# Optimization experiments

Measured on AMD Instinct MI355X. Metric: run time of the kernel, lower is better.

Reference implementation:

```python
import jax, jax.numpy as jnp
import numpy as np

N_EMBD = 1024
N_HEAD = 16
HEAD_DIM = N_EMBD // N_HEAD


def _linear_params(key, fan_in, fan_out):
    kw, kb = jax.random.split(key)
    bound = 1.0 / np.sqrt(fan_in)
    W = jax.random.uniform(kw, (fan_out, fan_in), minval=-bound, maxval=bound, dtype=jnp.float32)
    b = jax.random.uniform(kb, (fan_out,), minval=-bound, maxval=bound, dtype=jnp.float32)
    return W, b


def setup_inputs() -> dict:
    key = jax.random.key(0)
    ks = jax.random.split(key, 7)
    B, T, C = 4, 2048, N_EMBD
    k = jax.random.normal(ks[0], (B, T, C), dtype=jnp.float32)
    q = jax.random.normal(ks[1], (B, T, C), dtype=jnp.float32)
    v = jax.random.normal(ks[2], (B, T, C), dtype=jnp.float32)
    Wk, bk = _linear_params(ks[3], C, C)
    Wq, bq = _linear_params(ks[4], C, C)
    Wv, bv = _linear_params(ks[5], C, C)
    Wo, bo = _linear_params(ks[6], C, C)
    return {"k": k, "q": q, "v": v, "Wk": Wk, "bk": bk, "Wq": Wq, "bq": bq,
            "Wv": Wv, "bv": bv, "Wo": Wo, "bo": bo}


def reference(k, q, v, Wk, bk, Wq, bq, Wv, bv, Wo, bo):
    B, T, C = k.shape
    H, CH = N_HEAD, C // N_HEAD
    # projections (nn.Linear: x @ W.T + b), split heads -> [b, h, t, ch]
    keys = (k @ Wk.T + bk).reshape(B, T, H, CH).transpose(0, 2, 1, 3)
    queries = (q @ Wq.T + bq).reshape(B, T, H, CH).transpose(0, 2, 1, 3)
    values = (v @ Wv.T + bv).reshape(B, T, H, CH).transpose(0, 2, 1, 3)
    # [b, h, t, t] scores, scaled before softmax as in the original
    att = jnp.einsum('bhqd,bhkd->bhqk', queries, keys)
    att = jax.nn.softmax(att * (CH ** -0.5), axis=-1)
    out = jnp.einsum('bhqk,bhkd->bhqd', att, values)
    out = out.transpose(0, 2, 1, 3).reshape(B, T, C)
    return out @ Wo.T + bo
```

## Files before the change

### kernel.cpp

```cpp
#include <hip/hip_runtime.h>


typedef short bf8 __attribute__((ext_vector_type(8)));
typedef float f4 __attribute__((ext_vector_type(4)));
typedef float f16v __attribute__((ext_vector_type(16)));
typedef unsigned short u16;

#define AS1 __attribute__((address_space(1)))
#define AS3 __attribute__((address_space(3)))

__device__ __forceinline__ u16 f2b(float f) {
  unsigned u = __builtin_bit_cast(unsigned, f);
  u += 0x7FFFu + ((u >> 16) & 1u);
  return (u16)(u >> 16);
}

__device__ __forceinline__ unsigned cvtpk(float lo, float hi) {
  unsigned r;
  asm("v_cvt_pk_bf16_f32 %0, %1, %2" : "=v"(r) : "v"(lo), "v"(hi));
  return r;
}

__device__ __forceinline__ void swap32(unsigned& a, unsigned& b) {
  asm("v_permlane32_swap_b32 %0, %1" : "+v"(a), "+v"(b));
}

__global__ void cvt4_kernel(const float* __restrict__ a, const float* __restrict__ b,
                            const float* __restrict__ c, const float* __restrict__ d,
                            u16* __restrict__ out) {
  int i = blockIdx.x * blockDim.x + threadIdx.x;
  const int sel = i >> 18, off = i & 0x3FFFF;
  const float* src = sel == 0 ? a : sel == 1 ? b : sel == 2 ? c : d;
  float4 f = ((const float4*)src)[off];
  ushort4 o;
  o.x = f2b(f.x); o.y = f2b(f.y); o.z = f2b(f.z); o.w = f2b(f.w);
  ((ushort4*)out)[i] = o;
}

template<int MODE>
__device__ __forceinline__ void gemm_epilogue(
    f4 (&acc)[4][4], const float* __restrict__ bias, void* __restrict__ Cout,
    int N, float scale, int m0, int n0, int wm, int wn, int lr, int lg)
{
  if (MODE == 0) {
    float bv[4];
    #pragma unroll
    for (int j = 0; j < 4; ++j) bv[j] = bias[n0 + wn + j * 16 + lr];
    float* C = (float*)Cout;
    #pragma unroll
    for (int i = 0; i < 4; ++i)
      #pragma unroll
      for (int j = 0; j < 4; ++j) {
        const int col = n0 + wn + j * 16 + lr;
        #pragma unroll
        for (int r = 0; r < 4; ++r) {
          const int row = m0 + wm + i * 16 + lg * 4 + r;
          C[(size_t)row * N + col] = acc[i][j][r] + bv[j];
        }
      }
  } else if (MODE == 1) {
    float bv[4];
    #pragma unroll
    for (int j = 0; j < 4; ++j) bv[j] = bias[n0 + wn + j * 16 + lr];
    u16* C = (u16*)Cout;
    #pragma unroll
    for (int i = 0; i < 4; ++i)
      #pragma unroll
      for (int j = 0; j < 4; ++j) {
        const int col = n0 + wn + j * 16 + lr;
        const int h = col >> 6, ch = col & 63;
        #pragma unroll
        for (int r = 0; r < 4; ++r) {
          const int row = m0 + wm + i * 16 + lg * 4 + r;
          const int b = row >> 11, t = row & 2047;
          C[((size_t)(b * 16 + h) * 2048 + t) * 64 + ch] = f2b((acc[i][j][r] + bv[j]) * scale);
        }
      }
  } else {
    u16* C = (u16*)Cout;
    #pragma unroll
    for (int i = 0; i < 4; ++i)
      #pragma unroll
      for (int r = 0; r < 4; ++r) {
        const int nch = m0 + wm + i * 16 + lg * 4 + r;
        const float br = bias[nch];
        const int h = nch >> 6, ch = nch & 63;
        #pragma unroll
        for (int j = 0; j < 4; ++j) {
          const int tok = n0 + wn + j * 16 + lr;
          const int b = tok >> 11, t = tok & 2047;
          C[((size_t)((b * 16 + h) * 64 + ch) << 11) + t] = f2b(acc[i][j][r] + br);
        }
      }
  }
}

template<int MODE, int ACTB>
__device__ __forceinline__ void gemm_fp_body(
    u16* __restrict__ actT, u16* __restrict__ wT,
    const float* __restrict__ act, const u16* __restrict__ Wt,
    const float* __restrict__ bias, void* __restrict__ Cout,
    int N, int K, float scale, int m0, int n0)
{
  const int tid = threadIdx.x, lane = tid & 63, w = tid >> 6;
  const int wm = (w >> 1) << 6, wn = (w & 1) << 6;
  const int lr = lane & 15, lg = lane >> 4;
  const int arow0 = (ACTB ? n0 : m0);
  const int wrow0 = (ACTB ? m0 : n0);

  f4 acc[4][4] = {};
  float4 ta[8];

  #define W_GLDS(buf, karg)                                                     \
    do {                                                                        \
      const int k_ = (karg);                                                    \
      u16* dst = wT + ((buf) << 13);                                            \
      _Pragma("unroll")                                                         \
      for (int q = 0; q < 4; ++q) {                                             \
        const int c = (w << 8) + (q << 6) + lane;                               \
        const int row = c >> 3, sw = ((c & 7) ^ (row & 7)) << 3;                \
        __builtin_amdgcn_global_load_lds(                                       \
            (const AS1 void*)(Wt + (size_t)(wrow0 + row) * K + k_ + sw),        \
            (AS3 void*)(dst + (((w << 2) + q) << 9)), 16, 0, 0);                \
      }                                                                         \
    } while (0)

  #define ACT_LOAD(karg)                                                        \
    do {                                                                        \
      const int k_ = (karg);                                                    \
      _Pragma("unroll")                                                         \
      for (int q = 0; q < 4; ++q) {                                             \
        const int c = (w << 8) + (q << 6) + lane;                               \
        const int row = c >> 3, col = (c & 7) << 3;                             \
        const float* s = act + (size_t)(arow0 + row) * K + k_ + col;            \
        ta[2 * q] = *(const float4*)s;                                          \
        ta[2 * q + 1] = *(const float4*)(s + 4);                                \
      }                                                                         \
    } while (0)

  #define ACT_WRITE(buf)                                                        \
    do {                                                                        \
      u16* dst = actT + ((buf) << 13);                                          \
      _Pragma("unroll")                                                         \
      for (int q = 0; q < 4; ++q) {                                             \
        const int c = (w << 8) + (q << 6) + lane;                               \
        const int row = c >> 3;                                                 \
        uint4 pk;                                                               \
        pk.x = cvtpk(ta[2 * q].x, ta[2 * q].y);                                 \
        pk.y = cvtpk(ta[2 * q].z, ta[2 * q].w);                                 \
        pk.z = cvtpk(ta[2 * q + 1].x, ta[2 * q + 1].y);                         \
        pk.w = cvtpk(ta[2 * q + 1].z, ta[2 * q + 1].w);                         \
        *(uint4*)(dst + (row << 6) + (((c & 7) ^ (row & 7)) << 3)) = pk;        \
      }                                                                         \
    } while (0)

  W_GLDS(0, 0);
  ACT_LOAD(0);
  ACT_WRITE(0);
  ACT_LOAD(64);
  asm volatile("s_waitcnt lgkmcnt(0)" ::: "memory");

  const int NKT = K >> 6;
  for (int kt = 0; kt < NKT; ++kt) {
    const int cur = kt & 1;
    if (kt > 0) {
      if (kt + 1 < NKT) asm volatile("s_waitcnt vmcnt(8)" ::: "memory");
      else              asm volatile("s_waitcnt vmcnt(0)" ::: "memory");
    }
    __builtin_amdgcn_s_barrier();
    __builtin_amdgcn_sched_barrier(0);

    if (kt + 1 < NKT) W_GLDS(cur ^ 1, (kt + 1) << 6);

    const u16* aC = actT + (cur << 13);
    const u16* wC = wT + (cur << 13);
    #pragma unroll
    for (int ks = 0; ks < 2; ++ks) {
      bf8 af[4], bfr[4];
      #pragma unroll
      for (int i = 0; i < 4; ++i) {
        const int ra = wm + i * 16 + lr;
        const int rb = wn + i * 16 + lr;
        const u16* aSrc = ACTB ? wC : aC;
        const u16* bSrc = ACTB ? aC : wC;
        af[i]  = *(const bf8*)(aSrc + (ra << 6) + ((((ks << 2) + lg) ^ (ra & 7)) << 3));
        bfr[i] = *(const bf8*)(bSrc + (rb << 6) + ((((ks << 2) + lg) ^ (rb & 7)) << 3));
      }
      __builtin_amdgcn_s_setprio(1);
      #pragma unroll
      for (int i = 0; i < 4; ++i)
        #pragma unroll
        for (int j = 0; j < 4; ++j)
          acc[i][j] = __builtin_amdgcn_mfma_f32_16x16x32_bf16(af[i], bfr[j], acc[i][j], 0, 0, 0);
      __builtin_amdgcn_s_setprio(0);
    }

    if (kt + 1 < NKT) {
      ACT_WRITE(cur ^ 1);
      if (kt + 2 < NKT) ACT_LOAD((kt + 2) << 6);
    }
    asm volatile("s_waitcnt lgkmcnt(0)" ::: "memory");
  }
  #undef W_GLDS
  #undef ACT_LOAD
  #undef ACT_WRITE

  gemm_epilogue<MODE>(acc, bias, Cout, N, scale, m0, n0, wm, wn, lr, lg);
}

__global__ __launch_bounds__(256, 2)
void proj_qkv(const float* __restrict__ q_in, const float* __restrict__ k_in,
              const float* __restrict__ v_in,
              const u16* __restrict__ Wq, const u16* __restrict__ Wk,
              const u16* __restrict__ Wv,
              const float* __restrict__ bq, const float* __restrict__ bk,
              const float* __restrict__ bv,
              u16* __restrict__ Qp, u16* __restrict__ Kp, u16* __restrict__ Vt,
              float qscale)
{
  __shared__ __align__(16) u16 pool[32768];
  u16* const actT = pool;
  u16* const wT   = pool + 16384;

  const int cpx = gridDim.x >> 3;
  const int bid = (blockIdx.x & 7) * cpx + (blockIdx.x >> 3);
  const int which = bid >> 9, sub = bid & 511;

  if (which < 2) {
    gemm_fp_body<1, 0>(actT, wT,
                       which ? k_in : q_in,
                       which ? Wk : Wq,
                       which ? bk : bq,
                       which ? (void*)Kp : (void*)Qp,
                       1024, 1024, which ? 1.f : qscale,
                       (sub >> 3) << 7, (sub & 7) << 7);
  } else {
    gemm_fp_body<2, 1>(actT, wT, v_in, Wv, bv, (void*)Vt,
                       8192, 1024, 1.f, (sub & 7) << 7, (sub >> 3) << 7);
  }
}

__global__ __launch_bounds__(256, 2)
void gemm_out(const u16* __restrict__ A, const u16* __restrict__ B,
              const float* __restrict__ bias, float* __restrict__ C)
{
  __shared__ __align__(16) u16 pool[32768];
  u16* const aT = pool;
  u16* const bT = pool + 16384;

  const int cpx = gridDim.x >> 3;
  const int bid = (blockIdx.x & 7) * cpx + (blockIdx.x >> 3);
  const int m0 = (bid >> 3) << 7, n0 = (bid & 7) << 7;
  const int tid = threadIdx.x, lane = tid & 63, w = tid >> 6;
  const int wm = (w >> 1) << 6, wn = (w & 1) << 6;
  const int lr = lane & 15, lg = lane >> 4;
  const int K = 1024;

  f4 acc[4][4] = {};

  #pragma unroll
  for (int q = 0; q < 4; ++q) {
    const int c = (w << 8) + (q << 6) + lane;
    const int row = c >> 3, sw = ((c & 7) ^ (row & 7)) << 3;
    __builtin_amdgcn_global_load_lds(
        (const AS1 void*)(A + (size_t)(m0 + row) * K + sw),
        (AS3 void*)(aT + (((w << 2) + q) << 9)), 16, 0, 0);
    __builtin_amdgcn_global_load_lds(
        (const AS1 void*)(B + (size_t)(n0 + row) * K + sw),
        (AS3 void*)(bT + (((w << 2) + q) << 9)), 16, 0, 0);
  }
  __syncthreads();

  for (int kt = 0; kt < 16; ++kt) {
    const int cur = kt & 1;
    const u16* aC = aT + (cur << 13);
    const u16* bC = bT + (cur << 13);
    if (kt + 1 < 16) {
      u16* aN = aT + ((cur ^ 1) << 13);
      u16* bN = bT + ((cur ^ 1) << 13);
      const int k1 = (kt + 1) << 6;
      #pragma unroll
      for (int q = 0; q < 4; ++q) {
        const int c = (w << 8) + (q << 6) + lane;
        const int row = c >> 3, sw = ((c & 7) ^ (row & 7)) << 3;
        __builtin_amdgcn_global_load_lds(
            (const AS1 void*)(A + (size_t)(m0 + row) * K + k1 + sw),
            (AS3 void*)(aN + (((w << 2) + q) << 9)), 16, 0, 0);
        __builtin_amdgcn_global_load_lds(
            (const AS1 void*)(B + (size_t)(n0 + row) * K + k1 + sw),
            (AS3 void*)(bN + (((w << 2) + q) << 9)), 16, 0, 0);
      }
    }
    #pragma unroll
    for (int ks = 0; ks < 2; ++ks) {
      bf8 af[4], bfr[4];
      #pragma unroll
      for (int i = 0; i < 4; ++i) {
        const int ra = wm + i * 16 + lr;
        const int rb = wn + i * 16 + lr;
        af[i]  = *(const bf8*)(aC + (ra << 6) + ((((ks << 2) + lg) ^ (ra & 7)) << 3));
        bfr[i] = *(const bf8*)(bC + (rb << 6) + ((((ks << 2) + lg) ^ (rb & 7)) << 3));
      }
      __builtin_amdgcn_s_setprio(1);
      #pragma unroll
      for (int i = 0; i < 4; ++i)
        #pragma unroll
        for (int j = 0; j < 4; ++j)
          acc[i][j] = __builtin_amdgcn_mfma_f32_16x16x32_bf16(af[i], bfr[j], acc[i][j], 0, 0, 0);
      __builtin_amdgcn_s_setprio(0);
    }
    __syncthreads();
  }

  gemm_epilogue<0>(acc, bias, (void*)C, 1024, 1.f, m0, n0, wm, wn, lr, lg);
}

__global__ __launch_bounds__(256, 3)
void attn_kernel(const u16* __restrict__ Qp, const u16* __restrict__ Kp,
                 const u16* __restrict__ VT, u16* __restrict__ Ob)
{
  __shared__ __align__(16) u16 pool[24576];
  u16* const ktb = pool;
  u16* const vtb = pool + 12288;

  const int flat = blockIdx.x;
  const int xcd = flat & 7, idx = flat >> 3;
  const int bh = (xcd << 3) + (idx >> 4);
  const int tq0 = (idx & 15) << 7;

  const int tid = threadIdx.x, lane = tid & 63, w = tid >> 6;
  const int ql = lane & 31, hi = lane >> 5;
  const size_t hoff = (size_t)bh * (2048 * 64);
  const u16* Kh = Kp + hoff;
  const u16* Vh = VT + hoff;

  bf8 qf[4];
  {
    const u16* qp_ = Qp + hoff + (size_t)(tq0 + w * 32 + ql) * 64 + hi * 8;
    #pragma unroll
    for (int ks = 0; ks < 4; ++ks) qf[ks] = *(const bf8*)(qp_ + 16 * ks);
  }

  f16v o0 = {}, o1 = {};
  float lrun = 0.f;

  const int c0i = (w << 7) + lane;
  const int c1i = c0i + 64;
  const int sr0 = c0i >> 3, ss0 = ((c0i & 7) ^ (sr0 & 7)) << 3;
  const int sr1 = c1i >> 3, ss1 = ((c1i & 7) ^ (sr1 & 7)) << 3;
  const int sd0 = (w << 10);
  const int sd1 = (w << 10) + 512;

  #define STAGE(buf, t0)                                                          \
    do {                                                                           \
      __builtin_amdgcn_global_load_lds((const AS1 void*)(Kh + (size_t)((t0) + sr0) * 64 + ss0), \
                                       (AS3 void*)(ktb + (buf) * 4096 + sd0), 16, 0, 0);  \
      __builtin_amdgcn_global_load_lds((const AS1 void*)(Kh + (size_t)((t0) + sr1) * 64 + ss1), \
                                       (AS3 void*)(ktb + (buf) * 4096 + sd1), 16, 0, 0);  \
      __builtin_amdgcn_global_load_lds((const AS1 void*)(Vh + (size_t)sr0 * 2048 + (t0) + ss0), \
                                       (AS3 void*)(vtb + (buf) * 4096 + sd0), 16, 0, 0);  \
      __builtin_amdgcn_global_load_lds((const AS1 void*)(Vh + (size_t)sr1 * 2048 + (t0) + ss1), \
                                       (AS3 void*)(vtb + (buf) * 4096 + sd1), 16, 0, 0);  \
    } while (0)

  STAGE(0, 0);
  STAGE(1, 64);

  const int xq = ql & 7;
  int bc = 0;
  for (int it = 0; it < 32; ++it) {
    if (it < 31) asm volatile("s_waitcnt vmcnt(4)" ::: "memory");
    else         asm volatile("s_waitcnt vmcnt(0)" ::: "memory");
    __builtin_amdgcn_s_barrier();
    __builtin_amdgcn_sched_barrier(0);

    if (it + 2 < 32) {
      const int bs = bc ? bc - 1 : 2;
      STAGE(bs, (it + 2) << 6);
    }

    const u16* kb = ktb + bc * 4096;
    const u16* vb = vtb + bc * 4096;

    f16v s0 = {}, s1 = {};
    #pragma unroll
    for (int ks = 0; ks < 4; ++ks) {
      bf8 kf0 = *(const bf8*)(kb + (ql << 6) + ((((ks << 1) + hi) ^ xq) << 3));
      bf8 kf1 = *(const bf8*)(kb + ((32 + ql) << 6) + ((((ks << 1) + hi) ^ xq) << 3));
      __builtin_amdgcn_s_setprio(1);
      s0 = __builtin_amdgcn_mfma_f32_32x32x16_bf16(kf0, qf[ks], s0, 0, 0, 0);
      s1 = __builtin_amdgcn_mfma_f32_32x32x16_bf16(kf1, qf[ks], s1, 0, 0, 0);
      __builtin_amdgcn_s_setprio(0);
    }

    bf8 vf0[4], vf1[4];
    #pragma unroll
    for (int ks = 0; ks < 4; ++ks) {
      vf0[ks] = *(const bf8*)(vb + (ql << 6) + ((((ks << 1) + hi) ^ xq) << 3));
      vf1[ks] = *(const bf8*)(vb + ((32 + ql) << 6) + ((((ks << 1) + hi) ^ xq) << 3));
    }

    float rs = 0.f;

    {
      unsigned wpk[8];
      #pragma unroll
      for (int i = 0; i < 8; ++i) {
        float e0 = __builtin_amdgcn_exp2f(s0[2 * i]);
        float e1 = __builtin_amdgcn_exp2f(s0[2 * i + 1]);
        rs += e0 + e1;
        wpk[i] = cvtpk(e0, e1);
      }
      swap32(wpk[0], wpk[2]); swap32(wpk[1], wpk[3]);
      swap32(wpk[4], wpk[6]); swap32(wpk[5], wpk[7]);
      bf8 pf0 = __builtin_bit_cast(bf8, make_uint4(wpk[0], wpk[1], wpk[2], wpk[3]));
      bf8 pf1 = __builtin_bit_cast(bf8, make_uint4(wpk[4], wpk[5], wpk[6], wpk[7]));
      __builtin_amdgcn_s_setprio(1);
      o0 = __builtin_amdgcn_mfma_f32_32x32x16_bf16(vf0[0], pf0, o0, 0, 0, 0);
      o1 = __builtin_amdgcn_mfma_f32_32x32x16_bf16(vf1[0], pf0, o1, 0, 0, 0);
      o0 = __builtin_amdgcn_mfma_f32_32x32x16_bf16(vf0[1], pf1, o0, 0, 0, 0);
      o1 = __builtin_amdgcn_mfma_f32_32x32x16_bf16(vf1[1], pf1, o1, 0, 0, 0);
      __builtin_amdgcn_s_setprio(0);
    }

    {
      unsigned wpk[8];
      #pragma unroll
      for (int i = 0; i < 8; ++i) {
        float e0 = __builtin_amdgcn_exp2f(s1[2 * i]);
        float e1 = __builtin_amdgcn_exp2f(s1[2 * i + 1]);
        rs += e0 + e1;
        wpk[i] = cvtpk(e0, e1);
      }
      swap32(wpk[0], wpk[2]); swap32(wpk[1], wpk[3]);
      swap32(wpk[4], wpk[6]); swap32(wpk[5], wpk[7]);
      bf8 pf2 = __builtin_bit_cast(bf8, make_uint4(wpk[0], wpk[1], wpk[2], wpk[3]));
      bf8 pf3 = __builtin_bit_cast(bf8, make_uint4(wpk[4], wpk[5], wpk[6], wpk[7]));
      __builtin_amdgcn_s_setprio(1);
      o0 = __builtin_amdgcn_mfma_f32_32x32x16_bf16(vf0[2], pf2, o0, 0, 0, 0);
      o1 = __builtin_amdgcn_mfma_f32_32x32x16_bf16(vf1[2], pf2, o1, 0, 0, 0);
      o0 = __builtin_amdgcn_mfma_f32_32x32x16_bf16(vf0[3], pf3, o0, 0, 0, 0);
      o1 = __builtin_amdgcn_mfma_f32_32x32x16_bf16(vf1[3], pf3, o1, 0, 0, 0);
      __builtin_amdgcn_s_setprio(0);
    }

    lrun += rs;
    bc = bc + 1 < 3 ? bc + 1 : 0;
  }
  #undef STAGE

  const float linv = 1.f / (lrun + __shfl_xor(lrun, 32));

  __syncthreads();
  u16* const ot = pool;
  const int orow = w * 32 + ql;
  #pragma unroll
  for (int c = 0; c < 2; ++c) {
    const f16v& o = c ? o1 : o0;
    #pragma unroll
    for (int g = 0; g < 4; ++g) {
      uint2 pk;
      pk.x = cvtpk(o[4 * g + 0] * linv, o[4 * g + 1] * linv);
      pk.y = cvtpk(o[4 * g + 2] * linv, o[4 * g + 3] * linv);
      *(uint2*)(ot + orow * 72 + 32 * c + 8 * g + 4 * hi) = pk;
    }
  }
  __syncthreads();

  const int b = bh >> 4, h = bh & 15;
  const int row = tid >> 1, seg = tid & 1;
  const u16* src = ot + row * 72 + seg * 32;
  u16* dst = Ob + ((size_t)(b * 2048 + tq0 + row) * 16 + h) * 64 + seg * 32;
  #pragma unroll
  for (int kk = 0; kk < 4; ++kk)
    *(uint4*)(dst + 8 * kk) = *(const uint4*)(src + 8 * kk);
}

extern "C" void kernel_launch(void* const* d_in, const int* in_sizes, int n_in,
                              void* d_out, int out_size, void* d_ws, size_t ws_size,
                              hipStream_t stream) {
  (void)in_sizes; (void)n_in; (void)out_size; (void)ws_size;
  const float* k_in = (const float*)d_in[0];
  const float* q_in = (const float*)d_in[1];
  const float* v_in = (const float*)d_in[2];
  const float* Wk = (const float*)d_in[3]; const float* bk = (const float*)d_in[4];
  const float* Wq = (const float*)d_in[5]; const float* bq = (const float*)d_in[6];
  const float* Wv = (const float*)d_in[7]; const float* bv = (const float*)d_in[8];
  const float* Wo = (const float*)d_in[9]; const float* bo = (const float*)d_in[10];
  float* out = (float*)d_out;

  char* ws = (char*)d_ws;
  const size_t SZ_ACT = (size_t)8192 * 1024 * 2;
  const size_t SZ_W   = (size_t)1024 * 1024 * 2;
  u16* Oc  = (u16*)(ws);
  u16* Qp  = (u16*)(ws + 1 * SZ_ACT);
  u16* Kp  = (u16*)(ws + 2 * SZ_ACT);
  u16* Vt  = (u16*)(ws + 3 * SZ_ACT);
  u16* Wqb = (u16*)(ws + 4 * SZ_ACT);
  u16* Wkb = (u16*)(ws + 4 * SZ_ACT + SZ_W);
  u16* Wvb = (u16*)(ws + 4 * SZ_ACT + 2 * SZ_W);
  u16* Wob = (u16*)(ws + 4 * SZ_ACT + 3 * SZ_W);

  cvt4_kernel<<<4096, 256, 0, stream>>>(Wq, Wk, Wv, Wo, Wqb);

  const float c0 = 0.125f * 1.4426950408889634f;

  proj_qkv<<<1536, 256, 0, stream>>>(q_in, k_in, v_in, Wqb, Wkb, Wvb,
                                     bq, bk, bv, Qp, Kp, Vt, c0);

  attn_kernel<<<1024, 256, 0, stream>>>(Qp, Kp, Vt, Oc);

  gemm_out<<<512, 256, 0, stream>>>(Oc, Wob, bo, out);
}
```

Measured before the change: 179.1 us.

## Shrink projection GEMM K-tile to 32 with triple-buffered LDS for higher occupancy

Reworks the fused QKV projection GEMM to use a K-tile of 32 instead of 64. It uses three LDS buffers instead of two, with a new 4-way swizzle and a new per-thread load mapping. LDS per block drops from 64KB to 48KB and the activation register staging is halved, so launch bounds go from 2 to 3 blocks per CU. The cost is twice as many barriers and K iterations, and less MFMA work between each synchronization.

```diff
diff --git a/kernel.cpp b/kernel.cpp
--- a/kernel.cpp
+++ b/kernel.cpp
@@ -107,84 +107,89 @@
   const int lr = lane & 15, lg = lane >> 4;
   const int arow0 = (ACTB ? n0 : m0);
   const int wrow0 = (ACTB ? m0 : n0);
+  const int aloc  = (ACTB ? wn : wm);
+  const int wloc  = (ACTB ? wm : wn);
 
   f4 acc[4][4] = {};
-  float4 ta[8];
+  float4 ta[4];
+
+  const int wq0row = (w << 5) + (lane >> 2);
+  const int wq1row = wq0row + 16;
+  const int wx = lane & 3;
+  const int ws0 = (wx ^ (wq0row & 3)) << 3;
+  const int ws1 = (wx ^ (wq1row & 3)) << 3;
+  const int wd0 = (w << 10);
+  const int wd1 = (w << 10) + 512;
+
+  const int ar   = tid >> 1;
+  const int axh  = (tid & 1) << 4;
+  const int ax0  = (tid & 1) << 1;
+  const int asw0 = ((ax0 ^ (ar & 3)) << 3);
+  const int asw1 = (((ax0 | 1) ^ (ar & 3)) << 3);
+  const int abase = ar << 5;
 
   #define W_GLDS(buf, karg)                                                     \
     do {                                                                        \
       const int k_ = (karg);                                                    \
-      u16* dst = wT + ((buf) << 13);                                            \
-      _Pragma("unroll")                                                         \
-      for (int q = 0; q < 4; ++q) {                                             \
-        const int c = (w << 8) + (q << 6) + lane;                               \
-        const int row = c >> 3, sw = ((c & 7) ^ (row & 7)) << 3;                \
-        __builtin_amdgcn_global_load_lds(                                       \
-            (const AS1 void*)(Wt + (size_t)(wrow0 + row) * K + k_ + sw),        \
-            (AS3 void*)(dst + (((w << 2) + q) << 9)), 16, 0, 0);                \
-      }                                                                         \
+      u16* dst = wT + (buf) * 4096;                                             \
+      __builtin_amdgcn_global_load_lds(                                         \
+          (const AS1 void*)(Wt + (size_t)(wrow0 + wq0row) * K + k_ + ws0),      \
+          (AS3 void*)(dst + wd0), 16, 0, 0);                                    \
+      __builtin_amdgcn_global_load_lds(                                         \
+          (const AS1 void*)(Wt + (size_t)(wrow0 + wq1row) * K + k_ + ws1),      \
+          (AS3 void*)(dst + wd1), 16, 0, 0);                                    \
     } while (0)
 
   #define ACT_LOAD(karg)                                                        \
     do {                                                                        \
-      const int k_ = (karg);                                                    \
-      _Pragma("unroll")                                                         \
-      for (int q = 0; q < 4; ++q) {                                             \
-        const int c = (w << 8) + (q << 6) + lane;                               \
-        const int row = c >> 3, col = (c & 7) << 3;                             \
-        const float* s = act + (size_t)(arow0 + row) * K + k_ + col;            \
-        ta[2 * q] = *(const float4*)s;                                          \
-        ta[2 * q + 1] = *(const float4*)(s + 4);                                \
-      }                                                                         \
+      const float* s = act + (size_t)(arow0 + ar) * K + (karg) + axh;           \
+      ta[0] = *(const float4*)(s);                                              \
+      ta[1] = *(const float4*)(s + 4);                                          \
+      ta[2] = *(const float4*)(s + 8);                                          \
+      ta[3] = *(const float4*)(s + 12);                                         \
     } while (0)
 
   #define ACT_WRITE(buf)                                                        \
     do {                                                                        \
-      u16* dst = actT + ((buf) << 13);                                          \
-      _Pragma("unroll")                                                         \
-      for (int q = 0; q < 4; ++q) {                                             \
-        const int c = (w << 8) + (q << 6) + lane;                               \
-        const int row = c >> 3;                                                 \
-        uint4 pk;                                                               \
-        pk.x = cvtpk(ta[2 * q].x, ta[2 * q].y);                                 \
-        pk.y = cvtpk(ta[2 * q].z, ta[2 * q].w);                                 \
-        pk.z = cvtpk(ta[2 * q + 1].x, ta[2 * q + 1].y);                         \
-        pk.w = cvtpk(ta[2 * q + 1].z, ta[2 * q + 1].w);                         \
-        *(uint4*)(dst + (row << 6) + (((c & 7) ^ (row & 7)) << 3)) = pk;        \
-      }                                                                         \
+      u16* dst = actT + (buf) * 4096 + abase;                                   \
+      uint4 pk0, pk1;                                                           \
+      pk0.x = cvtpk(ta[0].x, ta[0].y); pk0.y = cvtpk(ta[0].z, ta[0].w);         \
+      pk0.z = cvtpk(ta[1].x, ta[1].y); pk0.w = cvtpk(ta[1].z, ta[1].w);         \
+      pk1.x = cvtpk(ta[2].x, ta[2].y); pk1.y = cvtpk(ta[2].z, ta[2].w);         \
+      pk1.z = cvtpk(ta[3].x, ta[3].y); pk1.w = cvtpk(ta[3].z, ta[3].w);         \
+      *(uint4*)(dst + asw0) = pk0;                                              \
+      *(uint4*)(dst + asw1) = pk1;                                              \
     } while (0)
 
+  ACT_LOAD(0);
   W_GLDS(0, 0);
-  ACT_LOAD(0);
   ACT_WRITE(0);
-  ACT_LOAD(64);
+  ACT_LOAD(32);
   asm volatile("s_waitcnt lgkmcnt(0)" ::: "memory");
 
-  const int NKT = K >> 6;
+  const int NKT = K >> 5;
+  int bc = 0;
   for (int kt = 0; kt < NKT; ++kt) {
-    const int cur = kt & 1;
-    if (kt > 0) {
-      if (kt + 1 < NKT) asm volatile("s_waitcnt vmcnt(8)" ::: "memory");
-      else              asm volatile("s_waitcnt vmcnt(0)" ::: "memory");
-    }
+    if (kt + 1 < NKT) asm volatile("s_waitcnt vmcnt(4)" ::: "memory");
+    else              asm volatile("s_waitcnt vmcnt(0)" ::: "memory");
     __builtin_amdgcn_s_barrier();
     __builtin_amdgcn_sched_barrier(0);
 
-    if (kt + 1 < NKT) W_GLDS(cur ^ 1, (kt + 1) << 6);
-
-    const u16* aC = actT + (cur << 13);
-    const u16* wC = wT + (cur << 13);
-    #pragma unroll
-    for (int ks = 0; ks < 2; ++ks) {
+    const int bn = bc == 2 ? 0 : bc + 1;
+    if (kt + 1 < NKT) W_GLDS(bn, (kt + 1) << 5);
+
+    const u16* aC = actT + bc * 4096;
+    const u16* wC = wT + bc * 4096;
+    {
       bf8 af[4], bfr[4];
       #pragma unroll
       for (int i = 0; i < 4; ++i) {
-        const int ra = wm + i * 16 + lr;
-        const int rb = wn + i * 16 + lr;
-        const u16* aSrc = ACTB ? wC : aC;
-        const u16* bSrc = ACTB ? aC : wC;
-        af[i]  = *(const bf8*)(aSrc + (ra << 6) + ((((ks << 2) + lg) ^ (ra & 7)) << 3));
-        bfr[i] = *(const bf8*)(bSrc + (rb << 6) + ((((ks << 2) + lg) ^ (rb & 7)) << 3));
+        const int ral = aloc + i * 16 + lr;
+        const int rwl = wloc + i * 16 + lr;
+        const bf8 actf = *(const bf8*)(aC + (ral << 5) + ((lg ^ (ral & 3)) << 3));
+        const bf8 wf   = *(const bf8*)(wC + (rwl << 5) + ((lg ^ (rwl & 3)) << 3));
+        af[i]  = ACTB ? wf : actf;
+        bfr[i] = ACTB ? actf : wf;
       }
       __builtin_amdgcn_s_setprio(1);
       #pragma unroll
@@ -196,10 +201,11 @@
     }
 
     if (kt + 1 < NKT) {
-      ACT_WRITE(cur ^ 1);
-      if (kt + 2 < NKT) ACT_LOAD((kt + 2) << 6);
+      ACT_WRITE(bn);
+      if (kt + 2 < NKT) ACT_LOAD((kt + 2) << 5);
     }
     asm volatile("s_waitcnt lgkmcnt(0)" ::: "memory");
+    bc = bn;
   }
   #undef W_GLDS
   #undef ACT_LOAD
@@ -208,7 +214,7 @@
   gemm_epilogue<MODE>(acc, bias, Cout, N, scale, m0, n0, wm, wn, lr, lg);
 }
 
-__global__ __launch_bounds__(256, 2)
+__global__ __launch_bounds__(256, 3)
 void proj_qkv(const float* __restrict__ q_in, const float* __restrict__ k_in,
               const float* __restrict__ v_in,
               const u16* __restrict__ Wq, const u16* __restrict__ Wk,
@@ -218,9 +224,9 @@
               u16* __restrict__ Qp, u16* __restrict__ Kp, u16* __restrict__ Vt,
               float qscale)
 {
-  __shared__ __align__(16) u16 pool[32768];
+  __shared__ __align__(16) u16 pool[24576];
   u16* const actT = pool;
-  u16* const wT   = pool + 16384;
+  u16* const wT   = pool + 12288;
 
   const int cpx = gridDim.x >> 3;
   const int bid = (blockIdx.x & 7) * cpx + (blockIdx.x >> 3);
```

After: 188.9 us. +5.5%, slower.

## Software-pipeline QK^T of next tile with softmax/PV of current tile

Applied to the files above, without the earlier changes.

Restructures the attention inner loop so the QK^T MFMAs for tile t+1 are issued before the exp/pack/PV work for tile t, using ping-pong score registers unrolled by two. The goal is to overlap matrix-core work with the transcendental and permute work of the softmax. In exchange it holds two extra 32x32 accumulators, which raises register pressure at 3 waves per SIMD. It also now waits on vmcnt(0) every iteration, which weakens the overlap of global-to-LDS prefetch.

```diff
diff --git a/kernel.cpp b/kernel.cpp
--- a/kernel.cpp
+++ b/kernel.cpp
@@ -315,6 +315,72 @@
   gemm_epilogue<0>(acc, bias, (void*)C, 1024, 1.f, m0, n0, wm, wn, lr, lg);
 }
 
+__device__ __forceinline__ void qk_tile(const u16* kb, const bf8 (&qf)[4],
+                                        int ql, int hi, int xq, f16v& s0, f16v& s1) {
+  #pragma unroll
+  for (int ks = 0; ks < 4; ++ks) {
+    bf8 kf0 = *(const bf8*)(kb + (ql << 6) + ((((ks << 1) + hi) ^ xq) << 3));
+    bf8 kf1 = *(const bf8*)(kb + ((32 + ql) << 6) + ((((ks << 1) + hi) ^ xq) << 3));
+    __builtin_amdgcn_s_setprio(1);
+    s0 = __builtin_amdgcn_mfma_f32_32x32x16_bf16(kf0, qf[ks], s0, 0, 0, 0);
+    s1 = __builtin_amdgcn_mfma_f32_32x32x16_bf16(kf1, qf[ks], s1, 0, 0, 0);
+    __builtin_amdgcn_s_setprio(0);
+  }
+}
+
+__device__ __forceinline__ void sm_pv(f16v& s0v, f16v& s1v, const u16* vb,
+                                      int ql, int hi, int xq,
+                                      f16v& o0, f16v& o1, float& lrun) {
+  bf8 vf0[4], vf1[4];
+  #pragma unroll
+  for (int ks = 0; ks < 4; ++ks) {
+    vf0[ks] = *(const bf8*)(vb + (ql << 6) + ((((ks << 1) + hi) ^ xq) << 3));
+    vf1[ks] = *(const bf8*)(vb + ((32 + ql) << 6) + ((((ks << 1) + hi) ^ xq) << 3));
+  }
+  float rs = 0.f;
+  {
+    unsigned wpk[8];
+    #pragma unroll
+    for (int i = 0; i < 8; ++i) {
+      float e0 = __builtin_amdgcn_exp2f(s0v[2 * i]);
+      float e1 = __builtin_amdgcn_exp2f(s0v[2 * i + 1]);
+      rs += e0 + e1;
+      wpk[i] = cvtpk(e0, e1);
+    }
+    swap32(wpk[0], wpk[2]); swap32(wpk[1], wpk[3]);
+    swap32(wpk[4], wpk[6]); swap32(wpk[5], wpk[7]);
+    bf8 pf0 = __builtin_bit_cast(bf8, make_uint4(wpk[0], wpk[1], wpk[2], wpk[3]));
+    bf8 pf1 = __builtin_bit_cast(bf8, make_uint4(wpk[4], wpk[5], wpk[6], wpk[7]));
+    __builtin_amdgcn_s_setprio(1);
+    o0 = __builtin_amdgcn_mfma_f32_32x32x16_bf16(vf0[0], pf0, o0, 0, 0, 0);
+    o1 = __builtin_amdgcn_mfma_f32_32x32x16_bf16(vf1[0], pf0, o1, 0, 0, 0);
+    o0 = __builtin_amdgcn_mfma_f32_32x32x16_bf16(vf0[1], pf1, o0, 0, 0, 0);
+    o1 = __builtin_amdgcn_mfma_f32_32x32x16_bf16(vf1[1], pf1, o1, 0, 0, 0);
+    __builtin_amdgcn_s_setprio(0);
+  }
+  {
+    unsigned wpk[8];
+    #pragma unroll
+    for (int i = 0; i < 8; ++i) {
+      float e0 = __builtin_amdgcn_exp2f(s1v[2 * i]);
+      float e1 = __builtin_amdgcn_exp2f(s1v[2 * i + 1]);
+      rs += e0 + e1;
+      wpk[i] = cvtpk(e0, e1);
+    }
+    swap32(wpk[0], wpk[2]); swap32(wpk[1], wpk[3]);
+    swap32(wpk[4], wpk[6]); swap32(wpk[5], wpk[7]);
+    bf8 pf2 = __builtin_bit_cast(bf8, make_uint4(wpk[0], wpk[1], wpk[2], wpk[3]));
+    bf8 pf3 = __builtin_bit_cast(bf8, make_uint4(wpk[4], wpk[5], wpk[6], wpk[7]));
+    __builtin_amdgcn_s_setprio(1);
+    o0 = __builtin_amdgcn_mfma_f32_32x32x16_bf16(vf0[2], pf2, o0, 0, 0, 0);
+    o1 = __builtin_amdgcn_mfma_f32_32x32x16_bf16(vf1[2], pf2, o1, 0, 0, 0);
+    o0 = __builtin_amdgcn_mfma_f32_32x32x16_bf16(vf0[3], pf3, o0, 0, 0, 0);
+    o1 = __builtin_amdgcn_mfma_f32_32x32x16_bf16(vf1[3], pf3, o1, 0, 0, 0);
+    __builtin_amdgcn_s_setprio(0);
+  }
+  lrun += rs;
+}
+
 __global__ __launch_bounds__(256, 3)
 void attn_kernel(const u16* __restrict__ Qp, const u16* __restrict__ Kp,
                  const u16* __restrict__ VT, u16* __restrict__ Ob)
@@ -342,6 +408,7 @@
   }
 
   f16v o0 = {}, o1 = {};
+  f16v sA0 = {}, sA1 = {}, sB0 = {}, sB1 = {};
   float lrun = 0.f;
 
   const int c0i = (w << 7) + lane;
@@ -363,90 +430,37 @@
                                        (AS3 void*)(vtb + (buf) * 4096 + sd1), 16, 0, 0);  \
     } while (0)
 
+  const int xq = ql & 7;
+
   STAGE(0, 0);
   STAGE(1, 64);
-
-  const int xq = ql & 7;
+  asm volatile("s_waitcnt vmcnt(4)" ::: "memory");
+  __builtin_amdgcn_s_barrier();
+  qk_tile(ktb, qf, ql, hi, xq, sA0, sA1);
+
   int bc = 0;
-  for (int it = 0; it < 32; ++it) {
-    if (it < 31) asm volatile("s_waitcnt vmcnt(4)" ::: "memory");
-    else         asm volatile("s_waitcnt vmcnt(0)" ::: "memory");
-    __builtin_amdgcn_s_barrier();
-    __builtin_amdgcn_sched_barrier(0);
-
-    if (it + 2 < 32) {
-      const int bs = bc ? bc - 1 : 2;
-      STAGE(bs, (it + 2) << 6);
-    }
-
-    const u16* kb = ktb + bc * 4096;
-    const u16* vb = vtb + bc * 4096;
-
-    f16v s0 = {}, s1 = {};
-    #pragma unroll
-    for (int ks = 0; ks < 4; ++ks) {
-      bf8 kf0 = *(const bf8*)(kb + (ql << 6) + ((((ks << 1) + hi) ^ xq) << 3));
-      bf8 kf1 = *(const bf8*)(kb + ((32 + ql) << 6) + ((((ks << 1) + hi) ^ xq) << 3));
-      __builtin_amdgcn_s_setprio(1);
-      s0 = __builtin_amdgcn_mfma_f32_32x32x16_bf16(kf0, qf[ks], s0, 0, 0, 0);
-      s1 = __builtin_amdgcn_mfma_f32_32x32x16_bf16(kf1, qf[ks], s1, 0, 0, 0);
-      __builtin_amdgcn_s_setprio(0);
-    }
-
-    bf8 vf0[4], vf1[4];
-    #pragma unroll
-    for (int ks = 0; ks < 4; ++ks) {
-      vf0[ks] = *(const bf8*)(vb + (ql << 6) + ((((ks << 1) + hi) ^ xq) << 3));
-      vf1[ks] = *(const bf8*)(vb + ((32 + ql) << 6) + ((((ks << 1) + hi) ^ xq) << 3));
-    }
-
-    float rs = 0.f;
-
-    {
-      unsigned wpk[8];
-      #pragma unroll
-      for (int i = 0; i < 8; ++i) {
-        float e0 = __builtin_amdgcn_exp2f(s0[2 * i]);
-        float e1 = __builtin_amdgcn_exp2f(s0[2 * i + 1]);
-        rs += e0 + e1;
-        wpk[i] = cvtpk(e0, e1);
-      }
-      swap32(wpk[0], wpk[2]); swap32(wpk[1], wpk[3]);
-      swap32(wpk[4], wpk[6]); swap32(wpk[5], wpk[7]);
-      bf8 pf0 = __builtin_bit_cast(bf8, make_uint4(wpk[0], wpk[1], wpk[2], wpk[3]));
-      bf8 pf1 = __builtin_bit_cast(bf8, make_uint4(wpk[4], wpk[5], wpk[6], wpk[7]));
-      __builtin_amdgcn_s_setprio(1);
-      o0 = __builtin_amdgcn_mfma_f32_32x32x16_bf16(vf0[0], pf0, o0, 0, 0, 0);
-      o1 = __builtin_amdgcn_mfma_f32_32x32x16_bf16(vf1[0], pf0, o1, 0, 0, 0);
-      o0 = __builtin_amdgcn_mfma_f32_32x32x16_bf16(vf0[1], pf1, o0, 0, 0, 0);
-      o1 = __builtin_amdgcn_mfma_f32_32x32x16_bf16(vf1[1], pf1, o1, 0, 0, 0);
-      __builtin_amdgcn_s_setprio(0);
-    }
-
-    {
-      unsigned wpk[8];
-      #pragma unroll
-      for (int i = 0; i < 8; ++i) {
-        float e0 = __builtin_amdgcn_exp2f(s1[2 * i]);
-        float e1 = __builtin_amdgcn_exp2f(s1[2 * i + 1]);
-        rs += e0 + e1;
-        wpk[i] = cvtpk(e0, e1);
-      }
-      swap32(wpk[0], wpk[2]); swap32(wpk[1], wpk[3]);
-      swap32(wpk[4], wpk[6]); swap32(wpk[5], wpk[7]);
-      bf8 pf2 = __builtin_bit_cast(bf8, make_uint4(wpk[0], wpk[1], wpk[2], wpk[3]));
-      bf8 pf3 = __builtin_bit_cast(bf8, make_uint4(wpk[4], wpk[5], wpk[6], wpk[7]));
-      __builtin_amdgcn_s_setprio(1);
-      o0 = __builtin_amdgcn_mfma_f32_32x32x16_bf16(vf0[2], pf2, o0, 0, 0, 0);
-      o1 = __builtin_amdgcn_mfma_f32_32x32x16_bf16(vf1[2], pf2, o1, 0, 0, 0);
-      o0 = __builtin_amdgcn_mfma_f32_32x32x16_bf16(vf0[3], pf3, o0, 0, 0, 0);
-      o1 = __builtin_amdgcn_mfma_f32_32x32x16_bf16(vf1[3], pf3, o1, 0, 0, 0);
-      __builtin_amdgcn_s_setprio(0);
-    }
-
-    lrun += rs;
-    bc = bc + 1 < 3 ? bc + 1 : 0;
-  }
+  #define BODY(sc0, sc1, sn0, sn1, T)                                            \
+    do {                                                                          \
+      const int t_ = (T);                                                         \
+      asm volatile("s_waitcnt vmcnt(0)" ::: "memory");                            \
+      __builtin_amdgcn_s_barrier();                                               \
+      __builtin_amdgcn_sched_barrier(0);                                          \
+      const int bn_ = bc + 1 < 3 ? bc + 1 : 0;                                    \
+      const int bs_ = bn_ + 1 < 3 ? bn_ + 1 : 0;                                  \
+      if (t_ + 2 < 32) STAGE(bs_, (t_ + 2) << 6);                                 \
+      if (t_ + 1 < 32) {                                                          \
+        sn0 = (f16v){}; sn1 = (f16v){};                                           \
+        qk_tile(ktb + bn_ * 4096, qf, ql, hi, xq, sn0, sn1);                      \
+      }                                                                           \
+      sm_pv(sc0, sc1, vtb + bc * 4096, ql, hi, xq, o0, o1, lrun);                 \
+      bc = bn_;                                                                   \
+    } while (0)
+
+  for (int tt = 0; tt < 16; ++tt) {
+    BODY(sA0, sA1, sB0, sB1, 2 * tt);
+    BODY(sB0, sB1, sA0, sA1, 2 * tt + 1);
+  }
+  #undef BODY
   #undef STAGE
 
   const float linv = 1.f / (lrun + __shfl_xor(lrun, 32));
```

Result: no change. 179.3 us (+0.2%).

## Pre-convert activations to bf16 and unify projection GEMMs on direct LDS loads

Applied to the files above, without the earlier changes.

Adds a single conversion kernel that turns the q/k/v activations, as well as the weights, into bf16 workspace buffers. The QKV projection then loads both operands through global-to-LDS copies with a simple double-buffered loop, and shares one GEMM body with the output projection. This removes the in-register fp32 load-and-convert path and its custom waitcnt pipelining. In exchange it adds an extra full pass writing and re-reading the activations in bf16, and uses more workspace.

```diff
diff --git a/kernel.cpp b/kernel.cpp
--- a/kernel.cpp
+++ b/kernel.cpp
@@ -25,16 +25,30 @@
   asm("v_permlane32_swap_b32 %0, %1" : "+v"(a), "+v"(b));
 }
 
-__global__ void cvt4_kernel(const float* __restrict__ a, const float* __restrict__ b,
-                            const float* __restrict__ c, const float* __restrict__ d,
-                            u16* __restrict__ out) {
-  int i = blockIdx.x * blockDim.x + threadIdx.x;
-  const int sel = i >> 18, off = i & 0x3FFFF;
-  const float* src = sel == 0 ? a : sel == 1 ? b : sel == 2 ? c : d;
-  float4 f = ((const float4*)src)[off];
+__global__ void cvt_all(const float* __restrict__ q, const float* __restrict__ k,
+                        const float* __restrict__ v,
+                        const float* __restrict__ Wq_, const float* __restrict__ Wk_,
+                        const float* __restrict__ Wv_, const float* __restrict__ Wo_,
+                        u16* __restrict__ qb, u16* __restrict__ kb,
+                        u16* __restrict__ vb, u16* __restrict__ wb) {
+  const int i = blockIdx.x * blockDim.x + threadIdx.x;
+  float4 f;
   ushort4 o;
-  o.x = f2b(f.x); o.y = f2b(f.y); o.z = f2b(f.z); o.w = f2b(f.w);
-  ((ushort4*)out)[i] = o;
+  if (i < (1 << 20)) {
+    const int s = i >> 18, off = i & 0x3FFFF;
+    const float* src = s == 0 ? Wq_ : s == 1 ? Wk_ : s == 2 ? Wv_ : Wo_;
+    f = ((const float4*)src)[off];
+    o.x = f2b(f.x); o.y = f2b(f.y); o.z = f2b(f.z); o.w = f2b(f.w);
+    ((ushort4*)wb)[i] = o;
+  } else {
+    const int j = i - (1 << 20);
+    const int s = j >> 21, off = j & 0x1FFFFF;
+    const float* src = s == 0 ? q : s == 1 ? k : v;
+    u16* dst = s == 0 ? qb : s == 1 ? kb : vb;
+    f = ((const float4*)src)[off];
+    o.x = f2b(f.x); o.y = f2b(f.y); o.z = f2b(f.z); o.w = f2b(f.w);
+    ((ushort4*)dst)[off] = o;
+  }
 }
 
 template<int MODE>
@@ -95,85 +109,47 @@
   }
 }
 
-template<int MODE, int ACTB>
-__device__ __forceinline__ void gemm_fp_body(
-    u16* __restrict__ actT, u16* __restrict__ wT,
-    const float* __restrict__ act, const u16* __restrict__ Wt,
+template<int MODE>
+__device__ __forceinline__ void gemm_bf16_body(
+    u16* __restrict__ aT, u16* __restrict__ bT,
+    const u16* __restrict__ A, const u16* __restrict__ B,
     const float* __restrict__ bias, void* __restrict__ Cout,
     int N, int K, float scale, int m0, int n0)
 {
   const int tid = threadIdx.x, lane = tid & 63, w = tid >> 6;
   const int wm = (w >> 1) << 6, wn = (w & 1) << 6;
   const int lr = lane & 15, lg = lane >> 4;
-  const int arow0 = (ACTB ? n0 : m0);
-  const int wrow0 = (ACTB ? m0 : n0);
 
   f4 acc[4][4] = {};
-  float4 ta[8];
-
-  #define W_GLDS(buf, karg)                                                     \
+
+  #define AB_STAGE(buf, karg)                                                   \
     do {                                                                        \
       const int k_ = (karg);                                                    \
-      u16* dst = wT + ((buf) << 13);                                            \
+      u16* da = aT + ((buf) << 13);                                             \
+      u16* db = bT + ((buf) << 13);                                             \
       _Pragma("unroll")                                                         \
       for (int q = 0; q < 4; ++q) {                                             \
         const int c = (w << 8) + (q << 6) + lane;                               \
         const int row = c >> 3, sw = ((c & 7) ^ (row & 7)) << 3;                \
         __builtin_amdgcn_global_load_lds(                                       \
-            (const AS1 void*)(Wt + (size_t)(wrow0 + row) * K + k_ + sw),        \
-            (AS3 void*)(dst + (((w << 2) + q) << 9)), 16, 0, 0);                \
+            (const AS1 void*)(A + (size_t)(m0 + row) * K + k_ + sw),            \
+            (AS3 void*)(da + (((w << 2) + q) << 9)), 16, 0, 0);                 \
+        __builtin_amdgcn_global_load_lds(                                       \
+            (const AS1 void*)(B + (size_t)(n0 + row) * K + k_ + sw),            \
+            (AS3 void*)(db + (((w << 2) + q) << 9)), 16, 0, 0);                 \
       }                                                                         \
     } while (0)
 
-  #define ACT_LOAD(karg)                                                        \
-    do {                                                                        \
-      const int k_ = (karg);                                                    \
-      _Pragma("unroll")                                                         \
-      for (int q = 0; q < 4; ++q) {                                             \
-        const int c = (w << 8) + (q << 6) + lane;                               \
-        const int row = c >> 3, col = (c & 7) << 3;                             \
-        const float* s = act + (size_t)(arow0 + row) * K + k_ + col;            \
-        ta[2 * q] = *(const float4*)s;                                          \
-        ta[2 * q + 1] = *(const float4*)(s + 4);                                \
-      }                                                                         \
-    } while (0)
-
-  #define ACT_WRITE(buf)                                                        \
-    do {                                                                        \
-      u16* dst = actT + ((buf) << 13);                                          \
-      _Pragma("unroll")                                                         \
-      for (int q = 0; q < 4; ++q) {                                             \
-        const int c = (w << 8) + (q << 6) + lane;                               \
-        const int row = c >> 3;                                                 \
-        uint4 pk;                                                               \
-        pk.x = cvtpk(ta[2 * q].x, ta[2 * q].y);                                 \
-        pk.y = cvtpk(ta[2 * q].z, ta[2 * q].w);                                 \
-        pk.z = cvtpk(ta[2 * q + 1].x, ta[2 * q + 1].y);                         \
-        pk.w = cvtpk(ta[2 * q + 1].z, ta[2 * q + 1].w);                         \
-        *(uint4*)(dst + (row << 6) + (((c & 7) ^ (row & 7)) << 3)) = pk;        \
-      }                                                                         \
-    } while (0)
-
-  W_GLDS(0, 0);
-  ACT_LOAD(0);
-  ACT_WRITE(0);
-  ACT_LOAD(64);
-  asm volatile("s_waitcnt lgkmcnt(0)" ::: "memory");
+  AB_STAGE(0, 0);
+  __syncthreads();
 
   const int NKT = K >> 6;
   for (int kt = 0; kt < NKT; ++kt) {
     const int cur = kt & 1;
-    if (kt > 0) {
-      if (kt + 1 < NKT) asm volatile("s_waitcnt vmcnt(8)" ::: "memory");
-      else              asm volatile("s_waitcnt vmcnt(0)" ::: "memory");
-    }
-    __builtin_amdgcn_s_barrier();
-    __builtin_amdgcn_sched_barrier(0);
-
-    if (kt + 1 < NKT) W_GLDS(cur ^ 1, (kt + 1) << 6);
-
-    const u16* aC = actT + (cur << 13);
-    const u16* wC = wT + (cur << 13);
+    const u16* aC = aT + (cur << 13);
+    const u16* bC = bT + (cur << 13);
+    if (kt + 1 < NKT) AB_STAGE(cur ^ 1, (kt + 1) << 6);
+
     #pragma unroll
     for (int ks = 0; ks < 2; ++ks) {
       bf8 af[4], bfr[4];
@@ -181,10 +157,8 @@
       for (int i = 0; i < 4; ++i) {
         const int ra = wm + i * 16 + lr;
         const int rb = wn + i * 16 + lr;
-        const u16* aSrc = ACTB ? wC : aC;
-        const u16* bSrc = ACTB ? aC : wC;
-        af[i]  = *(const bf8*)(aSrc + (ra << 6) + ((((ks << 2) + lg) ^ (ra & 7)) << 3));
-        bfr[i] = *(const bf8*)(bSrc + (rb << 6) + ((((ks << 2) + lg) ^ (rb & 7)) << 3));
+        af[i]  = *(const bf8*)(aC + (ra << 6) + ((((ks << 2) + lg) ^ (ra & 7)) << 3));
+        bfr[i] = *(const bf8*)(bC + (rb << 6) + ((((ks << 2) + lg) ^ (rb & 7)) << 3));
       }
       __builtin_amdgcn_s_setprio(1);
       #pragma unroll
@@ -194,23 +168,16 @@
           acc[i][j] = __builtin_amdgcn_mfma_f32_16x16x32_bf16(af[i], bfr[j], acc[i][j], 0, 0, 0);
       __builtin_amdgcn_s_setprio(0);
     }
-
-    if (kt + 1 < NKT) {
-      ACT_WRITE(cur ^ 1);
-      if (kt + 2 < NKT) ACT_LOAD((kt + 2) << 6);
-    }
-    asm volatile("s_waitcnt lgkmcnt(0)" ::: "memory");
-  }
-  #undef W_GLDS
-  #undef ACT_LOAD
-  #undef ACT_WRITE
+    __syncthreads();
+  }
+  #undef AB_STAGE
 
   gemm_epilogue<MODE>(acc, bias, Cout, N, scale, m0, n0, wm, wn, lr, lg);
 }
 
 __global__ __launch_bounds__(256, 2)
-void proj_qkv(const float* __restrict__ q_in, const float* __restrict__ k_in,
-              const float* __restrict__ v_in,
+void proj_qkv(const u16* __restrict__ qb, const u16* __restrict__ kb,
+              const u16* __restrict__ vb,
               const u16* __restrict__ Wq, const u16* __restrict__ Wk,
               const u16* __restrict__ Wv,
               const float* __restrict__ bq, const float* __restrict__ bk,
@@ -219,24 +186,24 @@
               float qscale)
 {
   __shared__ __align__(16) u16 pool[32768];
-  u16* const actT = pool;
-  u16* const wT   = pool + 16384;
+  u16* const aT = pool;
+  u16* const bT = pool + 16384;
 
   const int cpx = gridDim.x >> 3;
   const int bid = (blockIdx.x & 7) * cpx + (blockIdx.x >> 3);
   const int which = bid >> 9, sub = bid & 511;
 
   if (which < 2) {
-    gemm_fp_body<1, 0>(actT, wT,
-                       which ? k_in : q_in,
-                       which ? Wk : Wq,
-                       which ? bk : bq,
-                       which ? (void*)Kp : (void*)Qp,
-                       1024, 1024, which ? 1.f : qscale,
-                       (sub >> 3) << 7, (sub & 7) << 7);
+    gemm_bf16_body<1>(aT, bT,
+                      which ? kb : qb,
+                      which ? Wk : Wq,
+                      which ? bk : bq,
+                      which ? (void*)Kp : (void*)Qp,
+                      1024, 1024, which ? 1.f : qscale,
+                      (sub >> 3) << 7, (sub & 7) << 7);
   } else {
-    gemm_fp_body<2, 1>(actT, wT, v_in, Wv, bv, (void*)Vt,
-                       8192, 1024, 1.f, (sub & 7) << 7, (sub >> 3) << 7);
+    gemm_bf16_body<2>(aT, bT, Wv, vb, bv, (void*)Vt,
+                      8192, 1024, 1.f, (sub & 7) << 7, (sub >> 3) << 7);
   }
 }
 
@@ -250,69 +217,8 @@
 
   const int cpx = gridDim.x >> 3;
   const int bid = (blockIdx.x & 7) * cpx + (blockIdx.x >> 3);
-  const int m0 = (bid >> 3) << 7, n0 = (bid & 7) << 7;
-  const int tid = threadIdx.x, lane = tid & 63, w = tid >> 6;
-  const int wm = (w >> 1) << 6, wn = (w & 1) << 6;
-  const int lr = lane & 15, lg = lane >> 4;
-  const int K = 1024;
-
-  f4 acc[4][4] = {};
-
-  #pragma unroll
-  for (int q = 0; q < 4; ++q) {
-    const int c = (w << 8) + (q << 6) + lane;
-    const int row = c >> 3, sw = ((c & 7) ^ (row & 7)) << 3;
-    __builtin_amdgcn_global_load_lds(
-        (const AS1 void*)(A + (size_t)(m0 + row) * K + sw),
-        (AS3 void*)(aT + (((w << 2) + q) << 9)), 16, 0, 0);
-    __builtin_amdgcn_global_load_lds(
-        (const AS1 void*)(B + (size_t)(n0 + row) * K + sw),
-        (AS3 void*)(bT + (((w << 2) + q) << 9)), 16, 0, 0);
-  }
-  __syncthreads();
-
-  for (int kt = 0; kt < 16; ++kt) {
-    const int cur = kt & 1;
-    const u16* aC = aT + (cur << 13);
-    const u16* bC = bT + (cur << 13);
-    if (kt + 1 < 16) {
-      u16* aN = aT + ((cur ^ 1) << 13);
-      u16* bN = bT + ((cur ^ 1) << 13);
-      const int k1 = (kt + 1) << 6;
-      #pragma unroll
-      for (int q = 0; q < 4; ++q) {
-        const int c = (w << 8) + (q << 6) + lane;
-        const int row = c >> 3, sw = ((c & 7) ^ (row & 7)) << 3;
-        __builtin_amdgcn_global_load_lds(
-            (const AS1 void*)(A + (size_t)(m0 + row) * K + k1 + sw),
-            (AS3 void*)(aN + (((w << 2) + q) << 9)), 16, 0, 0);
-        __builtin_amdgcn_global_load_lds(
-            (const AS1 void*)(B + (size_t)(n0 + row) * K + k1 + sw),
-            (AS3 void*)(bN + (((w << 2) + q) << 9)), 16, 0, 0);
-      }
-    }
-    #pragma unroll
-    for (int ks = 0; ks < 2; ++ks) {
-      bf8 af[4], bfr[4];
-      #pragma unroll
-      for (int i = 0; i < 4; ++i) {
-        const int ra = wm + i * 16 + lr;
-        const int rb = wn + i * 16 + lr;
-        af[i]  = *(const bf8*)(aC + (ra << 6) + ((((ks << 2) + lg) ^ (ra & 7)) << 3));
-        bfr[i] = *(const bf8*)(bC + (rb << 6) + ((((ks << 2) + lg) ^ (rb & 7)) << 3));
-      }
-      __builtin_amdgcn_s_setprio(1);
-      #pragma unroll
-      for (int i = 0; i < 4; ++i)
-        #pragma unroll
-        for (int j = 0; j < 4; ++j)
-          acc[i][j] = __builtin_amdgcn_mfma_f32_16x16x32_bf16(af[i], bfr[j], acc[i][j], 0, 0, 0);
-      __builtin_amdgcn_s_setprio(0);
-    }
-    __syncthreads();
-  }
-
-  gemm_epilogue<0>(acc, bias, (void*)C, 1024, 1.f, m0, n0, wm, wn, lr, lg);
+  gemm_bf16_body<0>(aT, bT, A, B, bias, (void*)C, 1024, 1024, 1.f,
+                    (bid >> 3) << 7, (bid & 7) << 7);
 }
 
 __global__ __launch_bounds__(256, 3)
@@ -492,20 +398,24 @@
   char* ws = (char*)d_ws;
   const size_t SZ_ACT = (size_t)8192 * 1024 * 2;
   const size_t SZ_W   = (size_t)1024 * 1024 * 2;
-  u16* Oc  = (u16*)(ws);
-  u16* Qp  = (u16*)(ws + 1 * SZ_ACT);
-  u16* Kp  = (u16*)(ws + 2 * SZ_ACT);
-  u16* Vt  = (u16*)(ws + 3 * SZ_ACT);
-  u16* Wqb = (u16*)(ws + 4 * SZ_ACT);
-  u16* Wkb = (u16*)(ws + 4 * SZ_ACT + SZ_W);
-  u16* Wvb = (u16*)(ws + 4 * SZ_ACT + 2 * SZ_W);
-  u16* Wob = (u16*)(ws + 4 * SZ_ACT + 3 * SZ_W);
-
-  cvt4_kernel<<<4096, 256, 0, stream>>>(Wq, Wk, Wv, Wo, Wqb);
+  u16* qb  = (u16*)(ws);
+  u16* kb  = (u16*)(ws + 1 * SZ_ACT);
+  u16* vb  = (u16*)(ws + 2 * SZ_ACT);
+  u16* Qp  = (u16*)(ws + 3 * SZ_ACT);
+  u16* Kp  = (u16*)(ws + 4 * SZ_ACT);
+  u16* Vt  = (u16*)(ws + 5 * SZ_ACT);
+  u16* Wqb = (u16*)(ws + 6 * SZ_ACT);
+  u16* Wkb = (u16*)(ws + 6 * SZ_ACT + SZ_W);
+  u16* Wvb = (u16*)(ws + 6 * SZ_ACT + 2 * SZ_W);
+  u16* Wob = (u16*)(ws + 6 * SZ_ACT + 3 * SZ_W);
+  u16* Oc  = qb;
+
+  cvt_all<<<28672, 256, 0, stream>>>(q_in, k_in, v_in, Wq, Wk, Wv, Wo,
+                                     qb, kb, vb, Wqb);
 
   const float c0 = 0.125f * 1.4426950408889634f;
 
-  proj_qkv<<<1536, 256, 0, stream>>>(q_in, k_in, v_in, Wqb, Wkb, Wvb,
+  proj_qkv<<<1536, 256, 0, stream>>>(qb, kb, vb, Wqb, Wkb, Wvb,
                                      bq, bk, bv, Qp, Kp, Vt, c0);
 
   attn_kernel<<<1024, 256, 0, stream>>>(Qp, Kp, Vt, Oc);
```

Measured after the change: 188.4 us. 1.05x slower.
